# Kernel optimization log

Measured on AMD Instinct MI355X. Metric: run time of the kernel, lower is better.

Reference implementation:

```python
import jax, jax.numpy as jnp
import numpy as np

# regular 3x3 kernel grid: row0 = dy (i-1), row1 = dx (j-1), k = 3*i + j
RY = jnp.array([-1., -1., -1., 0., 0., 0., 1., 1., 1.], dtype=jnp.float32)
RX = jnp.array([-1., 0., 1., -1., 0., 1., -1., 0., 1.], dtype=jnp.float32)


def conv2d(x, w, b):
    # 3x3, stride 1, pad 1, NCHW/OIHW
    out = jax.lax.conv_general_dilated(
        x, w, window_strides=(1, 1), padding=((1, 1), (1, 1)),
        dimension_numbers=('NCHW', 'OIHW', 'NCHW'))
    return out + b[None, :, None, None]


def group_norm(x, gamma, beta, num_groups, eps=1e-5):
    N, C, H, W = x.shape
    xg = x.reshape(N, num_groups, C // num_groups, H, W)
    mu = xg.mean(axis=(2, 3, 4), keepdims=True)
    var = xg.var(axis=(2, 3, 4), keepdims=True)
    xn = ((xg - mu) * jax.lax.rsqrt(var + eps)).reshape(N, C, H, W)
    return xn * gamma[None, :, None, None] + beta[None, :, None, None]


def build_offset(tm, tr):
    # tm: [N,4,H,W] per-pixel 2x2 affine [[m00,m01],[m10,m11]]; tr: [N,2,H,W] (ty, tx)
    m00, m01, m10, m11 = tm[:, 0], tm[:, 1], tm[:, 2], tm[:, 3]  # [N,H,W]
    ry = RY[None, :, None, None]
    rx = RX[None, :, None, None]
    # offset = M @ R - R, plus translation broadcast to all 9 points
    dy = m00[:, None] * ry + m01[:, None] * rx - ry + tr[:, 0:1]  # [N,9,H,W]
    dx = m10[:, None] * ry + m11[:, None] * rx - rx + tr[:, 1:2]  # [N,9,H,W]
    return dy, dx


def bilinear_sample(img, py, px):
    # img: [N,C,H,W]; py, px: [N,K,H,W] sampling locations; zero padding outside
    N, C, H, W = img.shape
    K = py.shape[1]
    y0f = jnp.floor(py)
    x0f = jnp.floor(px)
    wy1 = py - y0f
    wx1 = px - x0f
    wy0 = 1.0 - wy1
    wx0 = 1.0 - wx1
    y0 = y0f.astype(jnp.int32)
    x0 = x0f.astype(jnp.int32)
    img_flat = img.reshape(N, C, H * W)

    def gather(yi, xi):
        valid = ((yi >= 0) & (yi < H) & (xi >= 0) & (xi < W)).astype(img.dtype)
        idx = jnp.clip(yi, 0, H - 1) * W + jnp.clip(xi, 0, W - 1)  # [N,K,H,W]
        flat = idx.reshape(N, 1, K * H * W)
        vals = jnp.take_along_axis(img_flat, jnp.broadcast_to(flat, (N, C, K * H * W)), axis=2)
        return vals.reshape(N, C, K, H, W) * valid[:, None]

    v00 = gather(y0, x0)
    v01 = gather(y0, x0 + 1)
    v10 = gather(y0 + 1, x0)
    v11 = gather(y0 + 1, x0 + 1)
    return (v00 * (wy0 * wx0)[:, None] + v01 * (wy0 * wx1)[:, None]
            + v10 * (wy1 * wx0)[:, None] + v11 * (wy1 * wx1)[:, None])


def deform_conv(x, dy, dx, w, pad=1, dil=1):
    # x: [N,Cin,H,W]; dy,dx: [N,9,H,W]; w: [Cout,Cin,3,3]; stride 1
    N, C, H, W = x.shape
    k = jnp.arange(9)
    ki = (k // 3).astype(x.dtype)[None, :, None, None]
    kj = (k % 3).astype(x.dtype)[None, :, None, None]
    hh = jnp.arange(H, dtype=x.dtype)[None, None, :, None]
    ww = jnp.arange(W, dtype=x.dtype)[None, None, None, :]
    py = hh - pad + dil * ki + dy  # [N,9,H,W]
    px = ww - pad + dil * kj + dx
    sampled = bilinear_sample(x, py, px)  # [N,C,9,H,W]
    return jnp.einsum('nckhw,ock->nohw', sampled, w.reshape(w.shape[0], C, 9))


def setup_inputs() -> dict:
    key = jax.random.key(0)
    ks = jax.random.split(key, 16)
    N, C, H, W = 4, 256, 64, 64
    x = jax.random.normal(ks[0], (N, C, H, W), jnp.float32)
    def p(k, shape, s):
        return jax.random.normal(k, shape, jnp.float32) * s
    s_off = 0.01                       # small STN heads -> modest offsets
    s_dc = 1.0 / np.sqrt(C * 9.0)      # deform-conv fan-in init
    return {
        'x': x,
        'w_tm1': p(ks[1], (4, C, 3, 3), s_off), 'b_tm1': jnp.zeros((4,), jnp.float32),
        'w_tr1': p(ks[2], (2, C, 3, 3), s_off), 'b_tr1': jnp.zeros((2,), jnp.float32),
        'w_dc1': p(ks[3], (C, C, 3, 3), s_dc),
        'g1': jnp.ones((C,), jnp.float32), 'be1': jnp.zeros((C,), jnp.float32),
        'w_tm2': p(ks[4], (4, C, 3, 3), s_off), 'b_tm2': jnp.zeros((4,), jnp.float32),
        'w_tr2': p(ks[5], (2, C, 3, 3), s_off), 'b_tr2': jnp.zeros((2,), jnp.float32),
        'w_dc2': p(ks[6], (C, C, 3, 3), s_dc),
        'g2': jnp.ones((C,), jnp.float32), 'be2': jnp.zeros((C,), jnp.float32),
    }


def reference(x, w_tm1, b_tm1, w_tr1, b_tr1, w_dc1, g1, be1,
              w_tm2, b_tm2, w_tr2, b_tr2, w_dc2, g2, be2):
    GROUPS = 32
    residual = x
    dy1, dx1 = build_offset(conv2d(x, w_tm1, b_tm1), conv2d(x, w_tr1, b_tr1))
    out = deform_conv(x, dy1, dx1, w_dc1)
    out = jax.nn.relu(group_norm(out, g1, be1, GROUPS))
    dy2, dx2 = build_offset(conv2d(out, w_tm2, b_tm2), conv2d(out, w_tr2, b_tr2))
    out = deform_conv(out, dy2, dx2, w_dc2)
    out = group_norm(out, g2, be2, GROUPS)
    return jax.nn.relu(out + residual)
```

## Files before the change

kernel.cpp:

```cpp
#include <hip/hip_runtime.h>


typedef unsigned int u32;
typedef unsigned short u16;
typedef __attribute__((ext_vector_type(8))) short bf16x8;
typedef __attribute__((ext_vector_type(4))) float floatx4;

#define HW 4096
#define CHW 1048576

static __device__ __forceinline__ float bf2f(u16 u) {
    union { u32 i; float f; } c; c.i = ((u32)u) << 16; return c.f;
}
static __device__ __forceinline__ u16 f2bf(float f) {
    union { float f; u32 i; } c; c.f = f;
    u32 x = c.i;
    return (u16)((x + 0x7FFFu + ((x >> 16) & 1u)) >> 16);
}
static __device__ __forceinline__ u32 cvtpk(float a, float b) {
    u32 r;
    asm("v_cvt_pk_bf16_f32 %0, %1, %2" : "=v"(r) : "v"(a), "v"(b));
    return r;
}
static __device__ __forceinline__ void lbar() {
    __builtin_amdgcn_sched_barrier(0);
    asm volatile("s_waitcnt lgkmcnt(0)" ::: "memory");
    __builtin_amdgcn_s_barrier();
    __builtin_amdgcn_sched_barrier(0);
}
static __device__ __forceinline__ float loadv(const void* p, long i, int f32) {
    return f32 ? ((const float*)p)[i] : bf2f(((const u16*)p)[i]);
}
static __device__ __forceinline__ int sniff_f32(const u32* __restrict__ xw) {
    int cnt = 0;
    #pragma unroll
    for (int s = 0; s < 16; ++s) {
        union { u32 i; float f; } c;
        c.i = xw[s * 131 + 7];
        float a = fabsf(c.f);
        if (a > 1e-8f && a < 1e4f) ++cnt;
    }
    return (cnt >= 8) ? 1 : 0;
}

__global__ __launch_bounds__(256) void k_prep_all(
    const void* __restrict__ x,
    const void* __restrict__ wdc1, const void* __restrict__ wdc2,
    const void* __restrict__ wtm1, const void* __restrict__ wtr1,
    const void* __restrict__ wtm2, const void* __restrict__ wtr2,
    u16* __restrict__ xT, u16* __restrict__ wTg1, u16* __restrict__ wTg2,
    u16* __restrict__ wT61, u16* __restrict__ wT62)
{
    __shared__ u16 T[64 * 258];
    const int f32 = sniff_f32((const u32*)x);
    const int b = blockIdx.x;
    const int tid = threadIdx.x;

    if (b < 256) {
        const int n = b >> 6, h = b & 63;
        const long sb = (long)n * CHW + (h << 6);
        const int cb = tid >> 3;
        const int w0 = (tid & 7) << 3;
        if (f32) {
            const float* xp = (const float*)x;
            for (int it = 0; it < 8; ++it) {
                int c = (it << 5) + cb;
                const float* pr = xp + sb + (long)c * HW + w0;
                float4 a = ((const float4*)pr)[0];
                float4 d = ((const float4*)pr)[1];
                T[(w0 + 0) * 258 + c] = f2bf(a.x);
                T[(w0 + 1) * 258 + c] = f2bf(a.y);
                T[(w0 + 2) * 258 + c] = f2bf(a.z);
                T[(w0 + 3) * 258 + c] = f2bf(a.w);
                T[(w0 + 4) * 258 + c] = f2bf(d.x);
                T[(w0 + 5) * 258 + c] = f2bf(d.y);
                T[(w0 + 6) * 258 + c] = f2bf(d.z);
                T[(w0 + 7) * 258 + c] = f2bf(d.w);
            }
        } else {
            const u16* xp = (const u16*)x;
            for (int it = 0; it < 8; ++it) {
                int c = (it << 5) + cb;
                uint4 v = *(const uint4*)(xp + sb + (long)c * HW + w0);
                u32 ws[4] = {v.x, v.y, v.z, v.w};
                #pragma unroll
                for (int q = 0; q < 4; ++q) {
                    T[(w0 + 2 * q + 0) * 258 + c] = (u16)(ws[q] & 0xFFFFu);
                    T[(w0 + 2 * q + 1) * 258 + c] = (u16)(ws[q] >> 16);
                }
            }
        }
        __syncthreads();
        const int w = tid >> 2, cq = tid & 3;
        const u32* Tr = (const u32*)T;
        u16* ob = xT + (long)n * CHW + (long)((h << 6) + w) * 256 + cq * 64;
        #pragma unroll
        for (int s = 0; s < 8; ++s) {
            uint4 o;
            o.x = Tr[129 * w + 32 * cq + 4 * s + 0];
            o.y = Tr[129 * w + 32 * cq + 4 * s + 1];
            o.z = Tr[129 * w + 32 * cq + 4 * s + 2];
            o.w = Tr[129 * w + 32 * cq + 4 * s + 3];
            *(uint4*)&ob[s * 8] = o;
        }
    } else if (b < 2560) {
        const int r2 = (b >= 1408);
        const void* wdc = r2 ? wdc2 : wdc1;
        u16* wTg = r2 ? wTg2 : wTg1;
        int idx2 = (b - (r2 ? 1408 : 256)) * 256 + tid;
        int cp = idx2 & 15;
        int o  = (idx2 >> 4) & 255;
        int q  = idx2 >> 12;
        int k  = q >> 3;
        int c0 = ((q & 7) << 5) + (cp << 1);
        long s0 = (long)o * 2304 + c0 * 9 + k;
        ((u32*)wTg)[idx2] = cvtpk(loadv(wdc, s0, f32), loadv(wdc, s0 + 9, f32));
    } else {
        const int r2 = (b >= 2704);
        const void* wtm = r2 ? wtm2 : wtm1;
        const void* wtr = r2 ? wtr2 : wtr1;
        u16* wT6 = r2 ? wT62 : wT61;
        int i = (b - (r2 ? 2704 : 2560)) * 256 + tid;
        int q  = i >> 9;
        int o  = (i >> 5) & 15;
        int cc = i & 31;
        int k  = q >> 3;
        int c  = ((q & 7) << 5) + cc;
        float v = 0.f;
        if (o < 4)      v = loadv(wtm, (long)o * 2304 + c * 9 + k, f32);
        else if (o < 6) v = loadv(wtr, (long)(o - 4) * 2304 + c * 9 + k, f32);
        wT6[i] = f2bf(v);
    }
}

__global__ __launch_bounds__(512, 4) void k_deform(
    const u16* __restrict__ srcT, const u16* __restrict__ wTg,
    const u16* __restrict__ wT6,
    const void* __restrict__ b_tm, const void* __restrict__ b_tr,
    const u32* __restrict__ xw,
    u16* __restrict__ raw, float* __restrict__ pstats)
{
    __shared__ float red[8][32][17];
    __shared__ float tl[6 * 32];
    __shared__ __align__(16) short Sl[2][32 * 40];
    __shared__ int   g_y0[288];
    __shared__ int   g_x0[288];
    __shared__ float g_wy[288];
    __shared__ float g_wx[288];

    const int tid = threadIdx.x;
    const int bid = blockIdx.x;
    const int n = bid >> 7, h = (bid >> 1) & 63, half = bid & 1;
    const int wb = half << 5;
    const int lane = tid & 63;
    const int quad = lane >> 4;
    const int l16  = lane & 15;
    const int wv   = tid >> 6;
    const long nbase = (long)n * CHW;
    const u16* sp = srcT + nbase;

    {
        floatx4 acc6[2];
        acc6[0] = (floatx4){0.f, 0.f, 0.f, 0.f};
        acc6[1] = (floatx4){0.f, 0.f, 0.f, 0.f};
        for (int qi = 0; qi < 9; ++qi) {
            const int q = wv * 9 + qi;
            const int k = q >> 3, cb = q & 7;
            const int ky = k / 3, kx = k % 3;
            const int row = h + ky - 1;
            const bool rv = (row >= 0) && (row < 64);
            bf16x8 av = *(const bf16x8*)&wT6[(((q << 4) + l16) << 5) + (quad << 3)];
            #pragma unroll
            for (int j = 0; j < 2; ++j) {
                int psrc = wb + (j << 4) + l16 + kx - 1;
                bf16x8 bv = {0, 0, 0, 0, 0, 0, 0, 0};
                if (rv && psrc >= 0 && psrc < 64)
                    bv = *(const bf16x8*)&sp[(((long)(row << 6) + psrc) << 8) + (cb << 5) + (quad << 3)];
                acc6[j] = __builtin_amdgcn_mfma_f32_16x16x32_bf16(av, bv, acc6[j], 0, 0, 0);
            }
        }
        #pragma unroll
        for (int j = 0; j < 2; ++j)
            #pragma unroll
            for (int r = 0; r < 4; ++r)
                red[wv][(j << 4) + l16][(quad << 2) + r] = acc6[j][r];
        __syncthreads();
        if (tid < 192) {
            const int o = tid >> 5, px = tid & 31;
            float s = 0.f;
            #pragma unroll
            for (int v = 0; v < 8; ++v) s += red[v][px][o];
            const int f32 = sniff_f32(xw);
            float bias = (o < 4) ? loadv(b_tm, o, f32) : loadv(b_tr, o - 4, f32);
            tl[o * 32 + px] = s + bias;
        }
        __syncthreads();
    }

    for (int i = tid; i < 288; i += 512) {
        int k = i >> 5, ww2 = i & 31;
        float m00 = tl[ww2],       m01 = tl[32 + ww2];
        float m10 = tl[64 + ww2],  m11 = tl[96 + ww2];
        float tr0 = tl[128 + ww2], tr1 = tl[160 + ww2];
        float ry = (float)(k / 3) - 1.f;
        float rx = (float)(k % 3) - 1.f;
        float dy = m00 * ry + m01 * rx - ry + tr0;
        float dx = m10 * ry + m11 * rx - rx + tr1;
        float py = (float)h + ry + dy;
        float px = (float)(wb + ww2) + rx + dx;
        float y0f = floorf(py), x0f = floorf(px);
        g_y0[i] = (int)y0f; g_x0[i] = (int)x0f;
        g_wy[i] = py - y0f; g_wx[i] = px - x0f;
    }
    __syncthreads();

    const int sw  = tid >> 4;
    const int scq = tid & 15;
    const int o0  = wv << 5;

    floatx4 acc[2][2];
    #pragma unroll
    for (int i = 0; i < 2; ++i)
        #pragma unroll
        for (int j = 0; j < 2; ++j)
            acc[i][j] = (floatx4){0.f, 0.f, 0.f, 0.f};

    short* slw = &Sl[0][sw * 40 + (scq << 1)];
    const short* slr = &Sl[0][l16 * 40 + (quad << 3)];
    const int wlane = ((o0 + l16) << 5) + (quad << 3);
    const u16* wq = wTg;

    const u16* p00; const u16* p01; const u16* p10; const u16* p11;
    float cw00, cw01, cw10, cw11;

    auto mkptr = [&](int k) {
        int gi = (k << 5) + sw;
        int y0 = g_y0[gi], x0 = g_x0[gi];
        int yc0 = min(max(y0, 0), 63),     yc1 = min(max(y0 + 1, 0), 63);
        int xc0 = min(max(x0, 0), 63),     xc1 = min(max(x0 + 1, 0), 63);
        const u16* bp = sp + (scq << 1);
        p00 = bp + (((yc0 << 6) + xc0) << 8);
        p01 = bp + (((yc0 << 6) + xc1) << 8);
        p10 = bp + (((yc1 << 6) + xc0) << 8);
        p11 = bp + (((yc1 << 6) + xc1) << 8);
    };
    auto mkcw = [&](int k) {
        int gi = (k << 5) + sw;
        int y0 = g_y0[gi], x0 = g_x0[gi];
        float wy1 = g_wy[gi], wx1 = g_wx[gi];
        float wy0 = 1.f - wy1, wx0 = 1.f - wx1;
        bool yv0 = (y0 >= 0) && (y0 < 64);
        bool yv1 = (y0 >= -1) && (y0 < 63);
        bool xv0 = (x0 >= 0) && (x0 < 64);
        bool xv1 = (x0 >= -1) && (x0 < 63);
        cw00 = (yv0 && xv0) ? wy0 * wx0 : 0.f;
        cw01 = (yv0 && xv1) ? wy0 * wx1 : 0.f;
        cw10 = (yv1 && xv0) ? wy1 * wx0 : 0.f;
        cw11 = (yv1 && xv1) ? wy1 * wx1 : 0.f;
    };

    u32 S[4][4];
    bf16x8 W0[4], W1[4];

    auto SMP = [&](int cb, int set) {
        S[set][0] = *(const u32*)(p00 + (cb << 5));
        S[set][1] = *(const u32*)(p01 + (cb << 5));
        S[set][2] = *(const u32*)(p10 + (cb << 5));
        S[set][3] = *(const u32*)(p11 + (cb << 5));
    };
    auto WLD = [&](int slot) {
        W0[slot] = *(const bf16x8*)(wq + wlane);
        W1[slot] = *(const bf16x8*)(wq + wlane + 512);
        wq += 8192;
    };
    auto PUB = [&](int set, int slot) {
        u32 r00 = S[set][0], r01 = S[set][1], r10 = S[set][2], r11 = S[set][3];
        float va = fmaf(cw00, bf2f((u16)r00),
                   fmaf(cw01, bf2f((u16)r01),
                   fmaf(cw10, bf2f((u16)r10), cw11 * bf2f((u16)r11))));
        float vb = fmaf(cw00, bf2f((u16)(r00 >> 16)),
                   fmaf(cw01, bf2f((u16)(r01 >> 16)),
                   fmaf(cw10, bf2f((u16)(r10 >> 16)), cw11 * bf2f((u16)(r11 >> 16)))));
        *(u32*)(slw + slot * 1280) = cvtpk(va, vb);
    };
    auto MFMA4 = [&](int ws, bf16x8 b0, bf16x8 b1) {
        acc[0][0] = __builtin_amdgcn_mfma_f32_16x16x32_bf16(W0[ws], b0, acc[0][0], 0, 0, 0);
        acc[1][0] = __builtin_amdgcn_mfma_f32_16x16x32_bf16(W1[ws], b0, acc[1][0], 0, 0, 0);
        acc[0][1] = __builtin_amdgcn_mfma_f32_16x16x32_bf16(W0[ws], b1, acc[0][1], 0, 0, 0);
        acc[1][1] = __builtin_amdgcn_mfma_f32_16x16x32_bf16(W1[ws], b1, acc[1][1], 0, 0, 0);
    };

    mkptr(0); mkcw(0);
    SMP(0, 0); SMP(1, 1); SMP(2, 2);
    WLD(0); WLD(1);
    PUB(0, 0);
    lbar();

    for (int k8 = 0; k8 < 8; ++k8) {
        #pragma unroll
        for (int c = 0; c < 8; ++c) {
            const int sl = c & 1;
            bf16x8 b0 = *(const bf16x8*)(slr + sl * 1280);
            bf16x8 b1 = *(const bf16x8*)(slr + sl * 1280 + 640);
            if (c == 5) mkptr(k8 + 1);
            SMP((c + 3) & 7, (c + 3) & 3);
            WLD((c + 2) & 3);
            if (c == 7) mkcw(k8 + 1);
            PUB((c + 1) & 3, (c + 1) & 1);
            MFMA4(c & 3, b0, b1);
            lbar();
        }
    }
    #pragma unroll
    for (int c = 0; c < 8; ++c) {
        const int sl = c & 1;
        bf16x8 b0 = *(const bf16x8*)(slr + sl * 1280);
        bf16x8 b1 = *(const bf16x8*)(slr + sl * 1280 + 640);
        if (c < 5) SMP((c + 3) & 7, (c + 3) & 3);
        if (c < 6) WLD((c + 2) & 3);
        if (c < 7) PUB((c + 1) & 3, (c + 1) & 1);
        MFMA4(c & 3, b0, b1);
        if (c < 7) lbar();
    }

    #pragma unroll
    for (int i = 0; i < 2; ++i) {
        float s1 = 0.f, s2 = 0.f;
        #pragma unroll
        for (int j = 0; j < 2; ++j)
            #pragma unroll
            for (int r = 0; r < 4; ++r) {
                float v = acc[i][j][r];
                s1 += v; s2 += v * v;
            }
        #pragma unroll
        for (int off = 1; off <= 16; off <<= 1) {
            s1 += __shfl_xor(s1, off, 64);
            s2 += __shfl_xor(s2, off, 64);
        }
        if ((lane & 31) == 0) {
            int g = (o0 >> 3) + 2 * i + (lane >> 5);
            pstats[((long)bid << 6) + (g << 1)]     = s1;
            pstats[((long)bid << 6) + (g << 1) + 1] = s2;
        }
    }

    #pragma unroll
    for (int i = 0; i < 2; ++i)
        #pragma unroll
        for (int j = 0; j < 2; ++j)
            #pragma unroll
            for (int r = 0; r < 4; ++r) {
                int o = o0 + i * 16 + quad * 4 + r;
                raw[nbase + ((long)o << 12) + (h << 6) + wb + (j << 4) + l16]
                    = f2bf(acc[i][j][r]);
            }
}

__global__ __launch_bounds__(256) void k_gn_relu(
    const u16* __restrict__ raw, const float* __restrict__ pstats,
    const void* __restrict__ gamma, const void* __restrict__ beta,
    const u32* __restrict__ xw,
    u16* __restrict__ out1)
{
    __shared__ u16 T[64 * 258];
    __shared__ float sred[4][64];
    __shared__ float sl[64];
    const int f32 = sniff_f32(xw);
    const int bid = blockIdx.x;
    const int n = bid >> 6, h = bid & 63;
    const int tid = threadIdx.x;

    {
        const int v = tid & 63, part = tid >> 6;
        float a = 0.f;
        for (int j = part * 32; j < part * 32 + 32; ++j)
            a += pstats[(((long)n * 128 + j) << 6) + v];
        sred[part][v] = a;
        __syncthreads();
        if (tid < 64) sl[tid] = sred[0][tid] + sred[1][tid] + sred[2][tid] + sred[3][tid];
        __syncthreads();
    }

    const u16* rb = raw + (long)n * CHW + (h << 6);
    const int cb = tid >> 3;
    const int w0 = (tid & 7) << 3;
    for (int it = 0; it < 8; ++it) {
        int c = (it << 5) + cb;
        int g = c >> 3;
        float mean = sl[g * 2] * (1.f / 32768.f);
        float var  = sl[g * 2 + 1] * (1.f / 32768.f) - mean * mean;
        float rstd = rsqrtf(var + 1e-5f);
        float ga = loadv(gamma, c, f32) * rstd;
        float be = loadv(beta, c, f32) - mean * ga;
        uint4 v = *(const uint4*)(rb + (long)c * HW + w0);
        u32 ws[4] = {v.x, v.y, v.z, v.w};
        #pragma unroll
        for (int q = 0; q < 4; ++q) {
            float a = fmaxf(fmaf(bf2f((u16)(ws[q] & 0xFFFFu)), ga, be), 0.f);
            float b = fmaxf(fmaf(bf2f((u16)(ws[q] >> 16)),     ga, be), 0.f);
            T[(w0 + 2 * q + 0) * 258 + c] = f2bf(a);
            T[(w0 + 2 * q + 1) * 258 + c] = f2bf(b);
        }
    }
    __syncthreads();
    const int w = tid >> 2, cq = tid & 3;
    const u32* Tr = (const u32*)T;
    u16* ob = out1 + (long)n * CHW + (long)((h << 6) + w) * 256 + cq * 64;
    #pragma unroll
    for (int s = 0; s < 8; ++s) {
        uint4 o;
        o.x = Tr[129 * w + 32 * cq + 4 * s + 0];
        o.y = Tr[129 * w + 32 * cq + 4 * s + 1];
        o.z = Tr[129 * w + 32 * cq + 4 * s + 2];
        o.w = Tr[129 * w + 32 * cq + 4 * s + 3];
        *(uint4*)&ob[s * 8] = o;
    }
}

__global__ __launch_bounds__(256) void k_gn_final(
    const u16* __restrict__ raw, const float* __restrict__ pstats,
    const void* __restrict__ gamma, const void* __restrict__ beta,
    const void* __restrict__ x,
    void* __restrict__ outp)
{
    __shared__ float rr[256];
    const int f32 = sniff_f32((const u32*)x);
    const int tid = threadIdx.x;
    const long e0 = ((long)blockIdx.x) << 11;
    const int n = (int)(e0 >> 20);
    const int c0 = (int)((e0 >> 12) & 255);
    const int g = c0 >> 3;

    {
        int j = tid & 127, sv = tid >> 7;
        rr[tid] = pstats[(((long)n * 128 + j) << 6) + (g << 1) + sv];
        __syncthreads();
        #pragma unroll
        for (int s = 64; s >= 1; s >>= 1) {
            if ((tid & 127) < s) rr[tid] += rr[tid + s];
            __syncthreads();
        }
    }
    float mean = rr[0] * (1.f / 32768.f);
    float var  = rr[128] * (1.f / 32768.f) - mean * mean;
    float rstd = rsqrtf(var + 1e-5f);

    const long i = blockIdx.x * 256 + tid;
    const long e = i << 3;
    const int c = (int)((e >> 12) & 255);
    float ga = loadv(gamma, c, f32) * rstd;
    float be = loadv(beta, c, f32) - mean * ga;
    uint4 p = ((const uint4*)raw)[i];
    u32 ww[4] = {p.x, p.y, p.z, p.w};
    float v[8];
    #pragma unroll
    for (int q = 0; q < 4; ++q) {
        v[2 * q + 0] = fmaxf(fmaf(bf2f((u16)(ww[q] & 0xFFFFu)), ga, be) + loadv(x, e + 2 * q + 0, f32), 0.f);
        v[2 * q + 1] = fmaxf(fmaf(bf2f((u16)(ww[q] >> 16)),     ga, be) + loadv(x, e + 2 * q + 1, f32), 0.f);
    }
    if (f32) {
        float4* op = (float4*)((float*)outp + e);
        op[0] = make_float4(v[0], v[1], v[2], v[3]);
        op[1] = make_float4(v[4], v[5], v[6], v[7]);
    } else {
        uint4 o;
        o.x = cvtpk(v[0], v[1]);
        o.y = cvtpk(v[2], v[3]);
        o.z = cvtpk(v[4], v[5]);
        o.w = cvtpk(v[6], v[7]);
        ((uint4*)outp)[i] = o;
    }
}

extern "C" void kernel_launch(void* const* d_in, const int* in_sizes, int n_in,
                              void* d_out, int out_size, void* d_ws, size_t ws_size,
                              hipStream_t stream) {
    const void* x     = d_in[0];
    const void* w_tm1 = d_in[1];
    const void* b_tm1 = d_in[2];
    const void* w_tr1 = d_in[3];
    const void* b_tr1 = d_in[4];
    const void* w_dc1 = d_in[5];
    const void* g1    = d_in[6];
    const void* be1   = d_in[7];
    const void* w_tm2 = d_in[8];
    const void* b_tm2 = d_in[9];
    const void* w_tr2 = d_in[10];
    const void* b_tr2 = d_in[11];
    const void* w_dc2 = d_in[12];
    const void* g2    = d_in[13];
    const void* be2   = d_in[14];

    char* wsb = (char*)d_ws;
    u16*   xT     = (u16*)wsb;
    u16*   raw    = (u16*)(wsb + 8388608);
    u16*   wTg1   = (u16*)(wsb + 16777216);
    u16*   wTg2   = (u16*)(wsb + 17956864);
    u16*   wT61   = (u16*)(wsb + 19136512);
    u16*   wT62   = (u16*)(wsb + 19210240);
    float* pstats = (float*)(wsb + 19283968);
    u16*   out1   = xT;
    const u32* xw = (const u32*)x;

    k_prep_all<<<2848, 256, 0, stream>>>(x, w_dc1, w_dc2, w_tm1, w_tr1, w_tm2, w_tr2,
                                         xT, wTg1, wTg2, wT61, wT62);
    k_deform  <<<512, 512, 0, stream>>>(xT, wTg1, wT61, b_tm1, b_tr1, xw, raw, pstats);
    k_gn_relu <<<256, 256, 0, stream>>>(raw, pstats, g1, be1, xw, out1);
    k_deform  <<<512, 512, 0, stream>>>(out1, wTg2, wT62, b_tm2, b_tr2, xw, raw, pstats);
    k_gn_final<<<2048, 256, 0, stream>>>(raw, pstats, g2, be2, x, d_out);
}
```

Before: 235.7 us.

## Stage full per-tap bilinear tile in swizzled LDS with 16-byte gathers

Replaces the per-32-channel-chunk sample/publish pipeline with one stage per kernel tap. Each thread gathers 16 channels per corner as wide 128-bit loads, bilinearly blends them, and writes the whole 256-channel tile into a double-buffered, XOR-swizzled LDS array. The MFMA loop then reads all 8 channel chunks from LDS with one barrier per tap instead of one per chunk. This cuts barrier count and the number of small 32-bit gathers, at the cost of much larger LDS use (32KB more) and more live registers, which may lower occupancy against the 512x4 launch bounds.

```diff
diff --git a/kernel.cpp b/kernel.cpp
--- a/kernel.cpp
+++ b/kernel.cpp
@@ -142,7 +142,7 @@
 {
     __shared__ float red[8][32][17];
     __shared__ float tl[6 * 32];
-    __shared__ __align__(16) short Sl[2][32 * 40];
+    __shared__ __align__(16) u32 Sl[2][4096];
     __shared__ int   g_y0[288];
     __shared__ int   g_x0[288];
     __shared__ float g_wy[288];
@@ -214,9 +214,12 @@
     }
     __syncthreads();
 
-    const int sw  = tid >> 4;
-    const int scq = tid & 15;
-    const int o0  = wv << 5;
+    const int px   = tid >> 4;
+    const int slot = tid & 15;
+    const int o0   = wv << 5;
+    const u32 xw_s = (u32)((px  & 7) << 2);
+    const u32 xsw  = (u32)((l16 & 7) << 2);
+    const u32 q4x  = (u32)(quad << 2);
 
     floatx4 acc[2][2];
     #pragma unroll
@@ -225,27 +228,25 @@
         for (int j = 0; j < 2; ++j)
             acc[i][j] = (floatx4){0.f, 0.f, 0.f, 0.f};
 
-    short* slw = &Sl[0][sw * 40 + (scq << 1)];
-    const short* slr = &Sl[0][l16 * 40 + (quad << 3)];
     const int wlane = ((o0 + l16) << 5) + (quad << 3);
     const u16* wq = wTg;
 
-    const u16* p00; const u16* p01; const u16* p10; const u16* p11;
+    const u16 *p00, *p01, *p10, *p11;
     float cw00, cw01, cw10, cw11;
 
     auto mkptr = [&](int k) {
-        int gi = (k << 5) + sw;
+        int gi = (k << 5) + px;
         int y0 = g_y0[gi], x0 = g_x0[gi];
         int yc0 = min(max(y0, 0), 63),     yc1 = min(max(y0 + 1, 0), 63);
         int xc0 = min(max(x0, 0), 63),     xc1 = min(max(x0 + 1, 0), 63);
-        const u16* bp = sp + (scq << 1);
+        const u16* bp = sp + (slot << 3);
         p00 = bp + (((yc0 << 6) + xc0) << 8);
         p01 = bp + (((yc0 << 6) + xc1) << 8);
         p10 = bp + (((yc1 << 6) + xc0) << 8);
         p11 = bp + (((yc1 << 6) + xc1) << 8);
     };
     auto mkcw = [&](int k) {
-        int gi = (k << 5) + sw;
+        int gi = (k << 5) + px;
         int y0 = g_y0[gi], x0 = g_x0[gi];
         float wy1 = g_wy[gi], wx1 = g_wx[gi];
         float wy0 = 1.f - wy1, wx0 = 1.f - wx1;
@@ -259,29 +260,19 @@
         cw11 = (yv1 && xv1) ? wy1 * wx1 : 0.f;
     };
 
-    u32 S[4][4];
+    uint4 GA, GB, GC, GD, HA, HB, HC, HD;
+    auto GATHER = [&]() {
+        GA = *(const uint4*)(p00);  HA = *(const uint4*)(p00 + 128);
+        GB = *(const uint4*)(p01);  HB = *(const uint4*)(p01 + 128);
+        GC = *(const uint4*)(p10);  HC = *(const uint4*)(p10 + 128);
+        GD = *(const uint4*)(p11);  HD = *(const uint4*)(p11 + 128);
+    };
+
     bf16x8 W0[4], W1[4];
-
-    auto SMP = [&](int cb, int set) {
-        S[set][0] = *(const u32*)(p00 + (cb << 5));
-        S[set][1] = *(const u32*)(p01 + (cb << 5));
-        S[set][2] = *(const u32*)(p10 + (cb << 5));
-        S[set][3] = *(const u32*)(p11 + (cb << 5));
-    };
-    auto WLD = [&](int slot) {
-        W0[slot] = *(const bf16x8*)(wq + wlane);
-        W1[slot] = *(const bf16x8*)(wq + wlane + 512);
+    auto WLD = [&](int s) {
+        W0[s] = *(const bf16x8*)(wq + wlane);
+        W1[s] = *(const bf16x8*)(wq + wlane + 512);
         wq += 8192;
-    };
-    auto PUB = [&](int set, int slot) {
-        u32 r00 = S[set][0], r01 = S[set][1], r10 = S[set][2], r11 = S[set][3];
-        float va = fmaf(cw00, bf2f((u16)r00),
-                   fmaf(cw01, bf2f((u16)r01),
-                   fmaf(cw10, bf2f((u16)r10), cw11 * bf2f((u16)r11))));
-        float vb = fmaf(cw00, bf2f((u16)(r00 >> 16)),
-                   fmaf(cw01, bf2f((u16)(r01 >> 16)),
-                   fmaf(cw10, bf2f((u16)(r10 >> 16)), cw11 * bf2f((u16)(r11 >> 16)))));
-        *(u32*)(slw + slot * 1280) = cvtpk(va, vb);
     };
     auto MFMA4 = [&](int ws, bf16x8 b0, bf16x8 b1) {
         acc[0][0] = __builtin_amdgcn_mfma_f32_16x16x32_bf16(W0[ws], b0, acc[0][0], 0, 0, 0);
@@ -290,38 +281,38 @@
         acc[1][1] = __builtin_amdgcn_mfma_f32_16x16x32_bf16(W1[ws], b1, acc[1][1], 0, 0, 0);
     };
 
-    mkptr(0); mkcw(0);
-    SMP(0, 0); SMP(1, 1); SMP(2, 2);
+#define BIL(a, b, c, d) cvtpk( \
+    fmaf(cw00, bf2f((u16)(a)), fmaf(cw01, bf2f((u16)(b)), \
+    fmaf(cw10, bf2f((u16)(c)), cw11 * bf2f((u16)(d))))), \
+    fmaf(cw00, bf2f((u16)((a) >> 16)), fmaf(cw01, bf2f((u16)((b) >> 16)), \
+    fmaf(cw10, bf2f((u16)((c) >> 16)), cw11 * bf2f((u16)((d) >> 16))))))
+
+    mkptr(0); GATHER();
     WLD(0); WLD(1);
-    PUB(0, 0);
-    lbar();
-
-    for (int k8 = 0; k8 < 8; ++k8) {
+
+    for (int k = 0; k < 9; ++k) {
+        const int buf = k & 1;
+        mkcw(k);
+        uint4 v0 = make_uint4(BIL(GA.x, GB.x, GC.x, GD.x), BIL(GA.y, GB.y, GC.y, GD.y),
+                              BIL(GA.z, GB.z, GC.z, GD.z), BIL(GA.w, GB.w, GC.w, GD.w));
+        uint4 v1 = make_uint4(BIL(HA.x, HB.x, HC.x, HD.x), BIL(HA.y, HB.y, HC.y, HD.y),
+                              BIL(HA.z, HB.z, HC.z, HD.z), BIL(HA.w, HB.w, HC.w, HD.w));
+        u32* wp = &Sl[buf][((u32)(px << 7)) + (((u32)(slot << 2)) ^ xw_s)];
+        *(uint4*)wp = v0;
+        *(uint4*)(wp + 64) = v1;
+        if (k < 8) { mkptr(k + 1); GATHER(); }
+        lbar();
+        const u32* sb = &Sl[buf][0];
         #pragma unroll
         for (int c = 0; c < 8; ++c) {
-            const int sl = c & 1;
-            bf16x8 b0 = *(const bf16x8*)(slr + sl * 1280);
-            bf16x8 b1 = *(const bf16x8*)(slr + sl * 1280 + 640);
-            if (c == 5) mkptr(k8 + 1);
-            SMP((c + 3) & 7, (c + 3) & 3);
-            WLD((c + 2) & 3);
-            if (c == 7) mkcw(k8 + 1);
-            PUB((c + 1) & 3, (c + 1) & 1);
+            const u32 offc = (((u32)(c << 4)) | q4x) ^ xsw;
+            bf16x8 b0 = *(const bf16x8*)(sb + ((u32)(l16 << 7)) + offc);
+            bf16x8 b1 = *(const bf16x8*)(sb + ((u32)((16 + l16) << 7)) + offc);
+            if (k < 8 || c < 6) WLD((c + 2) & 3);
             MFMA4(c & 3, b0, b1);
-            lbar();
-        }
-    }
-    #pragma unroll
-    for (int c = 0; c < 8; ++c) {
-        const int sl = c & 1;
-        bf16x8 b0 = *(const bf16x8*)(slr + sl * 1280);
-        bf16x8 b1 = *(const bf16x8*)(slr + sl * 1280 + 640);
-        if (c < 5) SMP((c + 3) & 7, (c + 3) & 3);
-        if (c < 6) WLD((c + 2) & 3);
-        if (c < 7) PUB((c + 1) & 3, (c + 1) & 1);
-        MFMA4(c & 3, b0, b1);
-        if (c < 7) lbar();
-    }
+        }
+    }
+#undef BIL
 
     #pragma unroll
     for (int i = 0; i < 2; ++i) {
```

Result: no change. 239.6 us (+1.7%).
